# Optimization experiments

Measured on AMD Instinct MI355X. Metric: run time of the kernel, lower is better.

Reference implementation:

```python
import jax, jax.numpy as jnp
import numpy as np

LIMIT_A = -0.1  # hard-concrete stretch lower limit
LIMIT_B = 1.1   # hard-concrete stretch upper limit
BATCH, IN_F, OUT_F = 64, 1024, 1024


def setup_inputs() -> dict:
    key = jax.random.key(0)
    kx, kw, kq = jax.random.split(key, 3)
    # fuzzy truth values in [0, 1]
    x = jax.random.uniform(kx, (BATCH, IN_F), dtype=jnp.float32)
    # Parameter(0.1 * torch.rand(in_features, out_features))
    weights = 0.1 * jax.random.uniform(kw, (IN_F, OUT_F), dtype=jnp.float32)
    # qz_loga init: normal(log(1-droprate)-log(droprate), 0.01) with droprate_init=0.5 -> mean 0
    qz_loga = 0.01 * jax.random.normal(kq, (IN_F,), dtype=jnp.float32)
    return {"x": x, "weights": weights, "qz_loga\u200b".replace("\u200b", ""): qz_loga}


def reference(x, weights, qz_loga):
    # Eval-mode L0ConjunctionLayer.forward (group_l0=True, randomly_binarize=False):
    #   z = hardtanh(sigmoid(qz_loga) * (limit_b - limit_a) + limit_a, 0, 1)  # (in,)
    #   w = z[:, None] * weights                                             # (in, out)
    #   out = prod_i (1 - (1 - x)[:, :, None] * w[None, :, :])               # (batch, out)
    pi = jax.nn.sigmoid(qz_loga)
    z = jnp.clip(pi * (LIMIT_B - LIMIT_A) + LIMIT_A, 0.0, 1.0)
    w = z[:, None] * weights  # (in, out)
    # fuzzy-AND gate: broadcast multiply then product-reduce over in_features
    out = jnp.prod(1.0 - (1.0 - x)[:, :, None] * w[None, :, :], axis=1)
    return out
```

## Files before the change

kernel.cpp:

```cpp
#include <hip/hip_runtime.h>


#define BATCH 64
#define IN_F  1024
#define OUT_F 1024

__global__ __launch_bounds__(256) void l0_fuzzy_and_main(
        const float* __restrict__ x,
        const float* __restrict__ w,
        const float* __restrict__ qz,
        float* __restrict__ outp,
        int L)
{
    extern __shared__ float u_lds[];
    const int bg = blockIdx.x;
    const int s  = blockIdx.y;
    const int i0 = s * L;
    const int b0 = bg * 4;
    const int t  = threadIdx.x;

    for (int idx = t; idx < L * 4; idx += 256) {
        const int ii = idx >> 2;
        const int bb = idx & 3;
        const int gi = i0 + ii;
        const float q  = qz[gi];
        const float pi = 1.0f / (1.0f + expf(-q));
        float z = fmaf(pi, 1.2f, -0.1f);
        z = fminf(fmaxf(z, 0.0f), 1.0f);
        const float xv = x[(b0 + bb) * IN_F + gi];
        u_lds[idx] = (1.0f - xv) * z;
    }
    __syncthreads();

    const int o = t * 4;
    float acc[4][4];
#pragma unroll
    for (int bb = 0; bb < 4; ++bb)
#pragma unroll
        for (int j = 0; j < 4; ++j)
            acc[bb][j] = 1.0f;

    const float* wp = w + (size_t)i0 * OUT_F + o;
#pragma unroll 4
    for (int ii = 0; ii < L; ++ii) {
        const float4 w4 = *(const float4*)wp;
        wp += OUT_F;
        const float4 u4 = *(const float4*)(&u_lds[ii * 4]);
        const float wv[4] = {w4.x, w4.y, w4.z, w4.w};
        const float uv[4] = {u4.x, u4.y, u4.z, u4.w};
#pragma unroll
        for (int bb = 0; bb < 4; ++bb)
#pragma unroll
            for (int j = 0; j < 4; ++j)
                acc[bb][j] *= fmaf(-uv[bb], wv[j], 1.0f);
    }

    float* op = outp + (size_t)(s * BATCH + b0) * OUT_F + o;
#pragma unroll
    for (int bb = 0; bb < 4; ++bb) {
        float4 v = make_float4(acc[bb][0], acc[bb][1], acc[bb][2], acc[bb][3]);
        *(float4*)(op + (size_t)bb * OUT_F) = v;
    }
}

__global__ __launch_bounds__(256) void l0_combine(
        const float* __restrict__ part, float* __restrict__ out, int S)
{
    const int idx = blockIdx.x * 256 + threadIdx.x;
    float p = 1.0f;
    for (int s = 0; s < S; ++s)
        p *= part[(size_t)s * (BATCH * OUT_F) + idx];
    out[idx] = p;
}

extern "C" void kernel_launch(void* const* d_in, const int* in_sizes, int n_in,
                              void* d_out, int out_size, void* d_ws, size_t ws_size,
                              hipStream_t stream)
{
    const float* x  = (const float*)d_in[0];
    const float* w  = (const float*)d_in[1];
    const float* qz = (const float*)d_in[2];
    float* out = (float*)d_out;

    int S = 16;
    while (S > 1 && (size_t)S * BATCH * OUT_F * sizeof(float) > ws_size)
        S >>= 1;
    const int L = IN_F / S;

    float* target = (S > 1) ? (float*)d_ws : out;
    dim3 grid(BATCH / 4, S);
    size_t lds_bytes = (size_t)L * 4 * sizeof(float);
    hipLaunchKernelGGL(l0_fuzzy_and_main, grid, dim3(256), lds_bytes, stream,
                       x, w, qz, target, L);

    if (S > 1) {
        hipLaunchKernelGGL(l0_combine, dim3((BATCH * OUT_F) / 256), dim3(256),
                           0, stream, (const float*)d_ws, out, S);
    }
}
```

Baseline: 73.75 us.

## Fuse split-K partials into single kernel with per-thread output columns

Replaces the split-over-inputs main kernel and its separate combine kernel with one kernel. Each block stages the gated inputs for 4 batch rows across the full input dimension in LDS. Each thread computes one output element over half the inputs and merges the two halves with a cross-lane shuffle. This removes the workspace partial writes and the second launch. In exchange it drops register blocking, so each thread issues one scalar weight load per multiply instead of one float4 load per 16 multiplies, which raises memory-instruction pressure.

```diff
diff --git a/kernel.cpp b/kernel.cpp
--- a/kernel.cpp
+++ b/kernel.cpp
@@ -1,76 +1,67 @@
 #include <hip/hip_runtime.h>
-
 
 #define BATCH 64
 #define IN_F  1024
 #define OUT_F 1024
 
-__global__ __launch_bounds__(256) void l0_fuzzy_and_main(
+__global__ __launch_bounds__(256) void l0_fuzzy_and_fused(
         const float* __restrict__ x,
         const float* __restrict__ w,
         const float* __restrict__ qz,
-        float* __restrict__ outp,
-        int L)
+        float* __restrict__ outp)
 {
-    extern __shared__ float u_lds[];
-    const int bg = blockIdx.x;
-    const int s  = blockIdx.y;
-    const int i0 = s * L;
-    const int b0 = bg * 4;
+    __shared__ float u_lds[4 * IN_F];
+
+    const int b0 = blockIdx.x * 4;
+    const int oc = blockIdx.y;
     const int t  = threadIdx.x;
 
-    for (int idx = t; idx < L * 4; idx += 256) {
-        const int ii = idx >> 2;
-        const int bb = idx & 3;
-        const int gi = i0 + ii;
-        const float q  = qz[gi];
+    for (int ii = t; ii < IN_F; ii += 256) {
+        const float q  = qz[ii];
         const float pi = 1.0f / (1.0f + expf(-q));
         float z = fmaf(pi, 1.2f, -0.1f);
         z = fminf(fmaxf(z, 0.0f), 1.0f);
-        const float xv = x[(b0 + bb) * IN_F + gi];
-        u_lds[idx] = (1.0f - xv) * z;
+#pragma unroll
+        for (int bb = 0; bb < 4; ++bb)
+            u_lds[bb * IN_F + ii] = (1.0f - x[(b0 + bb) * IN_F + ii]) * z;
     }
     __syncthreads();
 
-    const int o = t * 4;
-    float acc[4][4];
-#pragma unroll
-    for (int bb = 0; bb < 4; ++bb)
-#pragma unroll
-        for (int j = 0; j < 4; ++j)
-            acc[bb][j] = 1.0f;
+    const int ol = t & 31;
+    const int h  = (t >> 5) & 1;
+    const int bb = t >> 6;
+    const int o  = oc * 32 + ol;
 
-    const float* wp = w + (size_t)i0 * OUT_F + o;
+    const float* wp = w + (size_t)h * (IN_F / 2) * OUT_F + o;
+    const float* up = u_lds + bb * IN_F + h * (IN_F / 2);
+
+    float a0 = 1.0f, a1 = 1.0f, a2 = 1.0f, a3 = 1.0f;
 #pragma unroll 4
-    for (int ii = 0; ii < L; ++ii) {
-        const float4 w4 = *(const float4*)wp;
-        wp += OUT_F;
-        const float4 u4 = *(const float4*)(&u_lds[ii * 4]);
-        const float wv[4] = {w4.x, w4.y, w4.z, w4.w};
-        const float uv[4] = {u4.x, u4.y, u4.z, u4.w};
-#pragma unroll
-        for (int bb = 0; bb < 4; ++bb)
-#pragma unroll
-            for (int j = 0; j < 4; ++j)
-                acc[bb][j] *= fmaf(-uv[bb], wv[j], 1.0f);
+    for (int i = 0; i < IN_F / 2; i += 8) {
+        const float4 ua = *(const float4*)(up + i);
+        const float4 ub = *(const float4*)(up + i + 4);
+        const float w0 = wp[(size_t)(i + 0) * OUT_F];
+        const float w1 = wp[(size_t)(i + 1) * OUT_F];
+        const float w2 = wp[(size_t)(i + 2) * OUT_F];
+        const float w3 = wp[(size_t)(i + 3) * OUT_F];
+        const float w4 = wp[(size_t)(i + 4) * OUT_F];
+        const float w5 = wp[(size_t)(i + 5) * OUT_F];
+        const float w6 = wp[(size_t)(i + 6) * OUT_F];
+        const float w7 = wp[(size_t)(i + 7) * OUT_F];
+        a0 *= fmaf(-ua.x, w0, 1.0f);
+        a1 *= fmaf(-ua.y, w1, 1.0f);
+        a2 *= fmaf(-ua.z, w2, 1.0f);
+        a3 *= fmaf(-ua.w, w3, 1.0f);
+        a0 *= fmaf(-ub.x, w4, 1.0f);
+        a1 *= fmaf(-ub.y, w5, 1.0f);
+        a2 *= fmaf(-ub.z, w6, 1.0f);
+        a3 *= fmaf(-ub.w, w7, 1.0f);
     }
 
-    float* op = outp + (size_t)(s * BATCH + b0) * OUT_F + o;
-#pragma unroll
-    for (int bb = 0; bb < 4; ++bb) {
-        float4 v = make_float4(acc[bb][0], acc[bb][1], acc[bb][2], acc[bb][3]);
-        *(float4*)(op + (size_t)bb * OUT_F) = v;
-    }
-}
-
-__global__ __launch_bounds__(256) void l0_combine(
-        const float* __restrict__ part, float* __restrict__ out, int S)
-{
-    const int idx = blockIdx.x * 256 + threadIdx.x;
-    float p = 1.0f;
-    for (int s = 0; s < S; ++s)
-        p *= part[(size_t)s * (BATCH * OUT_F) + idx];
-    out[idx] = p;
+    float acc = (a0 * a1) * (a2 * a3);
+    acc *= __shfl_xor(acc, 32);
+    if (h == 0)
+        outp[(size_t)(b0 + bb) * OUT_F + o] = acc;
 }
 
 extern "C" void kernel_launch(void* const* d_in, const int* in_sizes, int n_in,
@@ -80,21 +71,8 @@
     const float* x  = (const float*)d_in[0];
     const float* w  = (const float*)d_in[1];
     const float* qz = (const float*)d_in[2];
-    float* out = (float*)d_out;
+    (void)d_ws; (void)ws_size;
 
-    int S = 16;
-    while (S > 1 && (size_t)S * BATCH * OUT_F * sizeof(float) > ws_size)
-        S >>= 1;
-    const int L = IN_F / S;
-
-    float* target = (S > 1) ? (float*)d_ws : out;
-    dim3 grid(BATCH / 4, S);
-    size_t lds_bytes = (size_t)L * 4 * sizeof(float);
-    hipLaunchKernelGGL(l0_fuzzy_and_main, grid, dim3(256), lds_bytes, stream,
-                       x, w, qz, target, L);
-
-    if (S > 1) {
-        hipLaunchKernelGGL(l0_combine, dim3((BATCH * OUT_F) / 256), dim3(256),
-                           0, stream, (const float*)d_ws, out, S);
-    }
+    hipLaunchKernelGGL(l0_fuzzy_and_fused, dim3(BATCH / 4, OUT_F / 32),
+                       dim3(256), 0, stream, x, w, qz, (float*)d_out);
 }
```

After: 73.97 us. Within noise of the previous version (+0.3%).
